# Performance work log

Hardware: AMD Instinct MI355X
Metric: run time of the kernel (lower is better)

The kernel has to match this reference:

```python
import jax, jax.numpy as jnp
import numpy as np
from jax import lax

B, T, L, D, K, VOCAB = 64, 128, 32, 128, 64, 50000


def setup_inputs() -> dict:
    key = jax.random.key(0)
    ks = jax.random.split(key, 8)
    prgrph = jax.random.randint(ks[0], (B, T, L), 0, VOCAB, dtype=jnp.int32)
    prgrph_mask = jax.random.randint(ks[1], (B, T, L), 0, 2, dtype=jnp.int32).astype(bool)
    embedding_matrix = jax.random.normal(ks[2], (VOCAB, D), dtype=jnp.float32)
    positional_mask = jax.random.normal(ks[3], (L, D), dtype=jnp.float32)
    Uw = jax.random.normal(ks[4], (D, D), dtype=jnp.float32) * 0.05
    Vw = jax.random.normal(ks[5], (D, D), dtype=jnp.float32) * 0.05
    Ww = jax.random.normal(ks[6], (D, D), dtype=jnp.float32) * 0.05
    keys = jax.random.normal(ks[7], (B, K, D), dtype=jnp.float32)
    return {"prgrph": prgrph, "prgrph_mask": prgrph_mask,
            "embedding_matrix": embedding_matrix, "positional_mask": positional_mask,
            "Uw": Uw, "Vw": Vw, "Ww": Ww, "keys": keys}


def _entity_scan(enc, sent_mask, keys, Uw, Vw, Ww):
    # enc: [B,T,D] encoded sentences; sent_mask: [B,T] bool; keys: [B,K,D]
    h0 = jnp.zeros_like(keys)  # initial entity hidden state = zeros

    def step(h, xs):
        s, m = xs  # s: [B,D], m: [B]
        # Eq 2: gate = sigmoid(s . h + s . k)  -> [B,K]
        g = jax.nn.sigmoid(jnp.einsum('bkd,bd->bk', h + keys, s))
        # Eq 3: h_tilda = sigmoid(h U + k V + s W)  -> [B,K,D]
        h_tilda = jax.nn.sigmoid(
            jnp.einsum('bkd,de->bke', h, Uw)
            + jnp.einsum('bkd,de->bke', keys, Vw)
            + (s @ Ww)[:, None, :])
        # Eq 4-5: add gated update, L2-normalize over embedding dim
        hn = h + g[..., None] * h_tilda
        hn = hn / jnp.sqrt(jnp.maximum(jnp.sum(hn * hn, axis=-1, keepdims=True), 1e-12))
        # only paragraphs with an active sentence at this step are updated
        h = jnp.where(m[:, None, None], hn, h)
        return h, None

    h_last, _ = lax.scan(step, h0, (jnp.swapaxes(enc, 0, 1), sent_mask.T))
    return h_last


def reference(prgrph, prgrph_mask, embedding_matrix, positional_mask, Uw, Vw, Ww, keys):
    # embed words; padded words contribute zero to the sentence encoding
    emb = embedding_matrix[prgrph] * prgrph_mask[..., None].astype(embedding_matrix.dtype)  # [B,T,L,D]
    # Sent_encoder: weighted bag of words with learned positional mask
    enc = jnp.einsum('btld,ld->btd', emb, positional_mask)  # [B,T,D]
    sent_mask = jnp.any(prgrph_mask, axis=2)  # [B,T]
    return _entity_scan(enc, sent_mask, keys, Uw, Vw, Ww)  # [B,K,D]
```

## Files before the change

kernel.cpp:

```cpp
#include <hip/hip_runtime.h>
#include <hip/hip_bf16.h>
#include <stdint.h>

#define B_ 64
#define T_ 128
#define L_ 32
#define D_ 128
#define K_ 64

#define FLAG_OFF 0
#define SM_OFF   256
#define ENC_OFF  (SM_OFF + B_*T_)
#define SW_OFF   (ENC_OFF + B_*T_*D_)
#define KS_OFF   (SW_OFF + B_*T_*D_)
#define KV_OFF   (KS_OFF + B_*T_*K_)

typedef __attribute__((ext_vector_type(8))) short short8b;
typedef __attribute__((ext_vector_type(4))) float f32x4;

union frag_cast { uint4 u; short8b s; };

__device__ __forceinline__ float sigmoidf_(float x){ return 1.0f/(1.0f + __expf(-x)); }

__device__ __forceinline__ unsigned short bfb(float x){
  __hip_bfloat16 h = __float2bfloat16(x);
  return __builtin_bit_cast(unsigned short, h);
}
__device__ __forceinline__ float bf2f(unsigned short u){
  return __uint_as_float(((unsigned)u) << 16);
}

__global__ __launch_bounds__(256) void k_detect(const uint8_t* __restrict__ m,
                                                int* __restrict__ flags){
  const unsigned* w = (const unsigned*)m;
  const int base = blockIdx.x * 512;
  unsigned acc = 0;
  acc |= w[base + threadIdx.x]       & 0xFFFFFF00u;
  acc |= w[base + threadIdx.x + 256] & 0xFFFFFF00u;
  int any = __syncthreads_or((int)(acc != 0u));
  if(threadIdx.x == 0) flags[blockIdx.x] = any;
}

__global__ __launch_bounds__(128) void k_enc(const int* __restrict__ prg,
                                             const uint8_t* __restrict__ pm8,
                                             const float* __restrict__ emb,
                                             const float* __restrict__ pos,
                                             const float* __restrict__ Ww,
                                             const float* __restrict__ keys,
                                             float* __restrict__ W){
  const int bt = blockIdx.x;
  const int b  = bt / T_;
  const int d  = threadIdx.x;
  int myf  = ((const int*)W)[FLAG_OFF + (d & 127)];
  int flag = __syncthreads_or(myf);
  __shared__ float keysl[K_*129];
  __shared__ float encl[D_];
  for(int r=0;r<K_;r++) keysl[r*129 + d] = keys[(b*K_ + r)*D_ + d];
  const int* pmi = (const int*)pm8;
  float acc = 0.f; int anym = 0;
  for(int l=0;l<L_;l++){
    int off = bt*L_ + l;
    int m = flag ? (int)pm8[off] : pmi[off];
    if(m){
      anym = 1;
      int idx = prg[off];
      acc += emb[idx*D_ + d] * pos[l*D_ + d];
    }
  }
  encl[d] = acc;
  W[ENC_OFF + bt*D_ + d] = acc;
  __syncthreads();
  float sw = 0.f;
  for(int e=0;e<D_;e++) sw += encl[e] * Ww[e*D_ + d];
  W[SW_OFF + bt*D_ + d] = sw;
  if(d < K_){
    float ks = 0.f;
    for(int dd=0;dd<D_;dd++) ks += keysl[d*129 + dd] * encl[dd];
    W[KS_OFF + bt*K_ + d] = ks;
  }
  if(d==0) W[SM_OFF + bt] = anym ? 1.f : 0.f;
}

__global__ __launch_bounds__(128) void k_kv(const float* __restrict__ keys,
                                            const float* __restrict__ Vw,
                                            float* __restrict__ W){
  const int bk = blockIdx.x;
  const int d  = threadIdx.x;
  __shared__ float kr[D_];
  kr[d] = keys[bk*D_ + d];
  __syncthreads();
  float acc = 0.f;
  for(int e=0;e<D_;e++) acc += kr[e] * Vw[e*D_ + d];
  W[KV_OFF + bk*D_ + d] = acc;
}

__global__ __launch_bounds__(64,1) void k_scan(const float* __restrict__ W,
                                               const float* __restrict__ Uw,
                                               float* __restrict__ out){
  const int b    = blockIdx.x >> 2;
  const int kg   = blockIdx.x & 3;
  const int lane = threadIdx.x;
  const int e    = lane & 15;
  const int q    = lane >> 4;

  short8b ufrag[8][4];
  #pragma unroll
  for(int rt=0; rt<8; ++rt){
    #pragma unroll
    for(int kc=0; kc<4; ++kc){
      const float* r0 = &Uw[(32*kc + 4*q)*D_ + 16*rt + e];
      short8b f;
      #pragma unroll
      for(int j=0;j<8;++j) f[j] = (short)bfb(r0[((j>>2)*16 + (j&3))*D_]);
      ufrag[rt][kc] = f;
    }
  }
  f32x4 kvv[8];
  {
    const float* kvp = &W[KV_OFF + (b*K_ + kg*16 + e)*D_ + 4*q];
    #pragma unroll
    for(int rt=0;rt<8;++rt) kvv[rt] = *(const f32x4*)&kvp[16*rt];
  }
  f32x4 vY[8];
  #pragma unroll
  for(int rt=0;rt<8;++rt) vY[rt] = 0.f;

  const float* ENC = &W[ENC_OFF + b*T_*D_];
  const float* SWg = &W[SW_OFF  + b*T_*D_];
  const float* KSg = &W[KS_OFF  + b*T_*K_];
  const float* SM  = &W[SM_OFF  + b*T_];

  auto loadstep = [&](int t, f32x4 (&sv)[8], f32x4 (&sk)[8], float& ks, float& sm){
    const float* sp = &ENC[t*D_ + 4*q];
    const float* wp = &SWg[t*D_ + 4*q];
    #pragma unroll
    for(int rt=0;rt<8;++rt){
      sv[rt] = *(const f32x4*)&sp[16*rt];
      f32x4 w = *(const f32x4*)&wp[16*rt];
      #pragma unroll
      for(int r=0;r<4;++r) sk[rt][r] = w[r] + kvv[rt][r];
    }
    ks = KSg[t*K_ + kg*16 + e];
    sm = SM[t];
  };

  auto cvt2 = [&](const f32x4& v, uint2& hi, uint2& lo){
    unsigned short h0=bfb(v[0]), h1=bfb(v[1]), h2=bfb(v[2]), h3=bfb(v[3]);
    hi.x = ((unsigned)h1<<16) | h0;
    hi.y = ((unsigned)h3<<16) | h2;
    unsigned short l0=bfb(v[0]-bf2f(h0)), l1=bfb(v[1]-bf2f(h1));
    unsigned short l2=bfb(v[2]-bf2f(h2)), l3=bfb(v[3]-bf2f(h3));
    lo.x = ((unsigned)l1<<16) | l0;
    lo.y = ((unsigned)l3<<16) | l2;
  };

  auto dostep = [&](const f32x4 (&sv)[8], const f32x4 (&skv)[8], float ks, float sm){
    if(sm != 0.f){
      short8b bhi[4], blo[4];
      #pragma unroll
      for(int kc=0;kc<4;++kc){
        uint2 ha, la, hb, lb;
        cvt2(vY[2*kc],   ha, la);
        cvt2(vY[2*kc+1], hb, lb);
        frag_cast fh; fh.u = make_uint4(ha.x, ha.y, hb.x, hb.y);
        frag_cast fl; fl.u = make_uint4(la.x, la.y, lb.x, lb.y);
        bhi[kc] = fh.s;
        blo[kc] = fl.s;
      }
      float ns = 0.f, gs = 0.f;
      #pragma unroll
      for(int rt=0;rt<8;++rt){
        #pragma unroll
        for(int r=0;r<4;++r){
          ns += vY[rt][r]*vY[rt][r];
          gs += vY[rt][r]*sv[rt][r];
        }
      }
      ns += __shfl_xor(ns,16);
      ns += __shfl_xor(ns,32);
      gs += __shfl_xor(gs,16);
      gs += __shfl_xor(gs,32);
      float n = rsqrtf(fmaxf(ns, 1e-12f));
      float g = sigmoidf_(fmaf(n, gs, ks));

      f32x4 acc[8];
      #pragma unroll
      for(int rt=0;rt<8;++rt) acc[rt] = 0.f;
      #pragma unroll
      for(int rt=0;rt<8;++rt){
        #pragma unroll
        for(int kc=0;kc<4;++kc){
          acc[rt] = __builtin_amdgcn_mfma_f32_16x16x32_bf16(ufrag[rt][kc], bhi[kc], acc[rt], 0,0,0);
          acc[rt] = __builtin_amdgcn_mfma_f32_16x16x32_bf16(ufrag[rt][kc], blo[kc], acc[rt], 0,0,0);
        }
      }

      #pragma unroll
      for(int rt=0;rt<8;++rt){
        #pragma unroll
        for(int r=0;r<4;++r){
          float x  = fmaf(n, acc[rt][r], skv[rt][r]);
          float ht = sigmoidf_(x);
          vY[rt][r] = fmaf(g, ht, n*vY[rt][r]);
        }
      }
    }
  };

  f32x4 svA[8], skA[8], svB[8], skB[8];
  float ksA, smA, ksB, smB;
  loadstep(0, svA, skA, ksA, smA);
  #pragma unroll 1
  for(int t=0; t<T_; t+=2){
    loadstep(t+1, svB, skB, ksB, smB);
    dostep(svA, skA, ksA, smA);
    int t2 = (t+2 < T_) ? (t+2) : 0;
    loadstep(t2, svA, skA, ksA, smA);
    dostep(svB, skB, ksB, smB);
  }

  float ns = 0.f;
  #pragma unroll
  for(int rt=0;rt<8;++rt){
    #pragma unroll
    for(int r=0;r<4;++r) ns += vY[rt][r]*vY[rt][r];
  }
  ns += __shfl_xor(ns,16);
  ns += __shfl_xor(ns,32);
  float n = rsqrtf(fmaxf(ns, 1e-12f));
  float* op = &out[(b*K_ + kg*16 + e)*D_ + 4*q];
  #pragma unroll
  for(int rt=0;rt<8;++rt){
    f32x4 o;
    #pragma unroll
    for(int r=0;r<4;++r) o[r] = vY[rt][r]*n;
    *(f32x4*)&op[16*rt] = o;
  }
}

extern "C" void kernel_launch(void* const* d_in, const int* in_sizes, int n_in,
                              void* d_out, int out_size, void* d_ws, size_t ws_size,
                              hipStream_t stream) {
  const int*     prg  = (const int*)d_in[0];
  const uint8_t* pm   = (const uint8_t*)d_in[1];
  const float*   emb  = (const float*)d_in[2];
  const float*   pos  = (const float*)d_in[3];
  const float*   Uw   = (const float*)d_in[4];
  const float*   Vw   = (const float*)d_in[5];
  const float*   Ww   = (const float*)d_in[6];
  const float*   keys = (const float*)d_in[7];
  float* W   = (float*)d_ws;
  float* out = (float*)d_out;

  hipLaunchKernelGGL(k_detect, dim3(128),    dim3(256), 0, stream, pm, (int*)d_ws + FLAG_OFF);
  hipLaunchKernelGGL(k_enc,    dim3(B_*T_),  dim3(128), 0, stream, prg, pm, emb, pos, Ww, keys, W);
  hipLaunchKernelGGL(k_kv,     dim3(B_*K_),  dim3(128), 0, stream, keys, Vw, W);
  hipLaunchKernelGGL(k_scan,   dim3(B_*4),   dim3(64),  0, stream, W, Uw, out);
}
```

Baseline: 515.6 us.

## Stage per-step scan inputs through an LDS ring buffer with deeper prefetch

Replaces the per-lane register double-buffer, in which every lane loaded all 128 enc and sW values per step, with a cooperative prefetch. Each lane loads one float4, the 64 lanes together covering enc and sW for one timestep, and commits it to an 8-slot shared-memory ring roughly 7-9 steps ahead. The step then reads its operands from LDS. This cuts redundant global loads and register pressure and hides global latency further ahead, at the cost of LDS reads on every step. The norm and gate reductions are also split into four independent accumulators to shorten the dependency chain.

```diff
diff --git a/kernel.cpp b/kernel.cpp
--- a/kernel.cpp
+++ b/kernel.cpp
@@ -103,6 +103,9 @@
   const int e    = lane & 15;
   const int q    = lane >> 4;
 
+  __shared__ float ring [8*256];
+  __shared__ float ringk[8*20];
+
   short8b ufrag[8][4];
   #pragma unroll
   for(int rt=0; rt<8; ++rt){
@@ -130,52 +133,63 @@
   const float* KSg = &W[KS_OFF  + b*T_*K_];
   const float* SM  = &W[SM_OFF  + b*T_];
 
-  auto loadstep = [&](int t, f32x4 (&sv)[8], f32x4 (&sk)[8], float& ks, float& sm){
-    const float* sp = &ENC[t*D_ + 4*q];
-    const float* wp = &SWg[t*D_ + 4*q];
-    #pragma unroll
-    for(int rt=0;rt<8;++rt){
-      sv[rt] = *(const f32x4*)&sp[16*rt];
-      f32x4 w = *(const f32x4*)&wp[16*rt];
-      #pragma unroll
-      for(int r=0;r<4;++r) sk[rt][r] = w[r] + kvv[rt][r];
-    }
-    ks = KSg[t*K_ + kg*16 + e];
-    sm = SM[t];
+  auto issue = [&](int t, f32x4& g, float& k, float& m){
+    int tL = (t < T_) ? t : (T_-1);
+    const float* src = (lane < 32) ? &ENC[tL*D_ + lane*4]
+                                   : &SWg[tL*D_ + (lane-32)*4];
+    g = *(const f32x4*)src;
+    k = KSg[tL*K_ + kg*16 + e];
+    m = SM[tL];
   };
-
-  auto cvt2 = [&](const f32x4& v, uint2& hi, uint2& lo){
-    unsigned short h0=bfb(v[0]), h1=bfb(v[1]), h2=bfb(v[2]), h3=bfb(v[3]);
-    hi.x = ((unsigned)h1<<16) | h0;
-    hi.y = ((unsigned)h3<<16) | h2;
-    unsigned short l0=bfb(v[0]-bf2f(h0)), l1=bfb(v[1]-bf2f(h1));
-    unsigned short l2=bfb(v[2]-bf2f(h2)), l3=bfb(v[3]-bf2f(h3));
-    lo.x = ((unsigned)l1<<16) | l0;
-    lo.y = ((unsigned)l3<<16) | l2;
+  auto commit = [&](int t, const f32x4& g, float k, float m){
+    int slot = t & 7;
+    *(f32x4*)&ring[slot*256 + lane*4] = g;
+    if(lane < 16)   ringk[slot*20 + lane] = k;
+    if(lane == 16)  ringk[slot*20 + 16]   = m;
   };
 
-  auto dostep = [&](const f32x4 (&sv)[8], const f32x4 (&skv)[8], float ks, float sm){
+  auto dostep = [&](int t, float sm){
     if(sm != 0.f){
+      int slot = t & 7;
+      f32x4 sv[8], sw[8];
+      #pragma unroll
+      for(int rt=0;rt<8;++rt){
+        sv[rt] = *(const f32x4*)&ring[slot*256 +       16*rt + 4*q];
+        sw[rt] = *(const f32x4*)&ring[slot*256 + 128 + 16*rt + 4*q];
+      }
+      float ks = ringk[slot*20 + e];
+
       short8b bhi[4], blo[4];
       #pragma unroll
       for(int kc=0;kc<4;++kc){
-        uint2 ha, la, hb, lb;
-        cvt2(vY[2*kc],   ha, la);
-        cvt2(vY[2*kc+1], hb, lb);
-        frag_cast fh; fh.u = make_uint4(ha.x, ha.y, hb.x, hb.y);
-        frag_cast fl; fl.u = make_uint4(la.x, la.y, lb.x, lb.y);
+        const f32x4& va = vY[2*kc];
+        const f32x4& vb = vY[2*kc+1];
+        unsigned short a0=bfb(va[0]), a1=bfb(va[1]), a2=bfb(va[2]), a3=bfb(va[3]);
+        unsigned short b0=bfb(vb[0]), b1=bfb(vb[1]), b2=bfb(vb[2]), b3=bfb(vb[3]);
+        frag_cast fh;
+        fh.u = make_uint4(((unsigned)a1<<16)|a0, ((unsigned)a3<<16)|a2,
+                          ((unsigned)b1<<16)|b0, ((unsigned)b3<<16)|b2);
+        unsigned short c0=bfb(va[0]-bf2f(a0)), c1=bfb(va[1]-bf2f(a1));
+        unsigned short c2=bfb(va[2]-bf2f(a2)), c3=bfb(va[3]-bf2f(a3));
+        unsigned short d0=bfb(vb[0]-bf2f(b0)), d1=bfb(vb[1]-bf2f(b1));
+        unsigned short d2=bfb(vb[2]-bf2f(b2)), d3=bfb(vb[3]-bf2f(b3));
+        frag_cast fl;
+        fl.u = make_uint4(((unsigned)c1<<16)|c0, ((unsigned)c3<<16)|c2,
+                          ((unsigned)d1<<16)|d0, ((unsigned)d3<<16)|d2);
         bhi[kc] = fh.s;
         blo[kc] = fl.s;
       }
-      float ns = 0.f, gs = 0.f;
-      #pragma unroll
-      for(int rt=0;rt<8;++rt){
-        #pragma unroll
-        for(int r=0;r<4;++r){
-          ns += vY[rt][r]*vY[rt][r];
-          gs += vY[rt][r]*sv[rt][r];
-        }
-      }
+
+      float n0=0.f,n1=0.f,n2=0.f,n3=0.f, g0=0.f,g1=0.f,g2=0.f,g3=0.f;
+      #pragma unroll
+      for(int rt=0;rt<8;++rt){
+        n0 += vY[rt][0]*vY[rt][0];  g0 += vY[rt][0]*sv[rt][0];
+        n1 += vY[rt][1]*vY[rt][1];  g1 += vY[rt][1]*sv[rt][1];
+        n2 += vY[rt][2]*vY[rt][2];  g2 += vY[rt][2]*sv[rt][2];
+        n3 += vY[rt][3]*vY[rt][3];  g3 += vY[rt][3]*sv[rt][3];
+      }
+      float ns = (n0+n1)+(n2+n3);
+      float gs = (g0+g1)+(g2+g3);
       ns += __shfl_xor(ns,16);
       ns += __shfl_xor(ns,32);
       gs += __shfl_xor(gs,16);
@@ -199,7 +213,7 @@
       for(int rt=0;rt<8;++rt){
         #pragma unroll
         for(int r=0;r<4;++r){
-          float x  = fmaf(n, acc[rt][r], skv[rt][r]);
+          float x  = fmaf(n, acc[rt][r], sw[rt][r] + kvv[rt][r]);
           float ht = sigmoidf_(x);
           vY[rt][r] = fmaf(g, ht, n*vY[rt][r]);
         }
@@ -207,16 +221,25 @@
     }
   };
 
-  f32x4 svA[8], skA[8], svB[8], skB[8];
-  float ksA, smA, ksB, smB;
-  loadstep(0, svA, skA, ksA, smA);
+  f32x4 gT; float kT, mT;
+  #pragma unroll 1
+  for(int s=0; s<7; ++s){ issue(s, gT, kT, mT); commit(s, gT, kT, mT); }
+  f32x4 gA, gB; float kA,kB,mA,mB;
+  issue(7, gA, kA, mA);
+  issue(8, gB, kB, mB);
+  float smC = ringk[0*20 + 16];
+
   #pragma unroll 1
   for(int t=0; t<T_; t+=2){
-    loadstep(t+1, svB, skB, ksB, smB);
-    dostep(svA, skA, ksA, smA);
-    int t2 = (t+2 < T_) ? (t+2) : 0;
-    loadstep(t2, svA, skA, ksA, smA);
-    dostep(svB, skB, ksB, smB);
+    commit(t+7, gA, kA, mA);
+    issue (t+9, gA, kA, mA);
+    float smN = ringk[((t+1)&7)*20 + 16];
+    dostep(t, smC);
+    commit(t+8, gB, kB, mB);
+    issue (t+10, gB, kB, mB);
+    float smN2 = ringk[((t+2)&7)*20 + 16];
+    dostep(t+1, smN);
+    smC = smN2;
   }
 
   float ns = 0.f;
```

New measurement: 487.2 us. -5.5%, faster.
